# Performance work log

Hardware: AMD Instinct MI355X
Metric: run time of the kernel (lower is better)

Reference implementation:

```python
import jax, jax.numpy as jnp
import numpy as np

N_NODES = 100000
N_EDGES = 1600000
D_FEAT = 64
POS_DIM = 3
D_HID = 64


def setup_inputs() -> dict:
    key = jax.random.key(0)
    ks = jax.random.split(key, 8)
    s = lambda fan_in: 1.0 / np.sqrt(fan_in)
    x = jax.random.normal(ks[0], (N_NODES, D_FEAT), dtype=jnp.float32)
    pos = jax.random.normal(ks[1], (N_NODES, POS_DIM), dtype=jnp.float32)
    edge_index = jax.random.randint(ks[2], (2, N_EDGES), 0, N_NODES, dtype=jnp.int64)
    d_msg_in = 2 * D_FEAT + POS_DIM  # 131
    d_agg_in = 2 * D_FEAT            # 128
    return {
        "x": x,
        "edge_index": edge_index,
        "pos": pos,
        "mw1": jax.random.normal(ks[3], (d_msg_in, D_HID), dtype=jnp.float32) * s(d_msg_in),
        "mb1": jnp.zeros((D_HID,), dtype=jnp.float32),
        "mw2": jax.random.normal(ks[4], (D_HID, D_HID), dtype=jnp.float32) * s(D_HID),
        "mb2": jnp.zeros((D_HID,), dtype=jnp.float32),
        "aw1": jax.random.normal(ks[5], (d_agg_in, D_HID), dtype=jnp.float32) * s(d_agg_in),
        "ab1": jnp.zeros((D_HID,), dtype=jnp.float32),
        "aw2": jax.random.normal(ks[6], (D_HID, D_HID), dtype=jnp.float32) * s(D_HID),
        "ab2": jnp.zeros((D_HID,), dtype=jnp.float32),
    }


def reference(x, edge_index, pos, mw1, mb1, mw2, mb2, aw1, ab1, aw2, ab2):
    # flow='target_to_source': aggregation node i = edge_index[0], neighbor j = edge_index[1]
    i = edge_index[0]
    j = edge_index[1]
    # message: msg_net(cat[x_i, x_j, pos_j - pos_i])   [E, 2d+pos]
    inp = jnp.concatenate([x[i], x[j], pos[j] - pos[i]], axis=1)
    h = jax.nn.relu(inp @ mw1 + mb1)
    msg = h @ mw2 + mb2  # [E, D_HID]
    n = x.shape[0]
    # scatter-mean aggregate at node i
    msg_sum = jax.ops.segment_sum(msg, i, num_segments=n)
    cnt = jax.ops.segment_sum(jnp.ones((i.shape[0], 1), x.dtype), i, num_segments=n)
    aggr = msg_sum / jnp.maximum(cnt, 1.0)
    # update: aggr_net(cat[x, aggr])  (self_val=True)
    u = jnp.concatenate([x, aggr], axis=1)
    return jax.nn.relu(u @ aw1 + ab1) @ aw2 + ab2
```

## Files before the change

### kernel.cpp

```cpp
#include <hip/hip_runtime.h>
#include <hip/hip_fp16.h>

#define N_NODES 100000
#define N_EDGES 1600000
#define NPART 98
#define CAP   20480
#define EB    8192

typedef _Float16 half8 __attribute__((ext_vector_type(8)));
typedef float f32x4 __attribute__((ext_vector_type(4)));

#define WS_OFF   0
#define WS_PCUR  400016
#define WS_B     400528
#define WS_SJ    401040
#define WS_WCOMB 6801040
#define WS_BCOMB 6817424
#define WS_PK    6817680
#define WS_QI8   6858640
#define WS_QS    13258640
#define WS_BIN   19658640
#define WS_HM16  19658640

__global__ void k_init0(int* pcur) {
    int t = threadIdx.x;
    if (t < NPART) pcur[t] = t * CAP;
}

__global__ void __launch_bounds__(256) k_binc(const int* __restrict__ ei,
                                              const int* __restrict__ ej,
                                              int* pcur, int* __restrict__ binned) {
    __shared__ int cnt[NPART];
    __shared__ int wcur[NPART];
    int t = threadIdx.x;
    for (int q = t; q < NPART; q += 256) cnt[q] = 0;
    __syncthreads();
    int base_e = blockIdx.x * EB;
    #pragma unroll 2
    for (int it = 0; it < EB / 1024; ++it) {
        int e = base_e + it * 1024 + t * 4;
        if (e < N_EDGES) {
            int4 iv = *(const int4*)(ei + e);
            atomicAdd(&cnt[iv.x >> 10], 1);
            atomicAdd(&cnt[iv.y >> 10], 1);
            atomicAdd(&cnt[iv.z >> 10], 1);
            atomicAdd(&cnt[iv.w >> 10], 1);
        }
    }
    __syncthreads();
    for (int q = t; q < NPART; q += 256)
        wcur[q] = cnt[q] ? atomicAdd(&pcur[q], cnt[q]) : 0;
    __syncthreads();
    #pragma unroll 2
    for (int it = 0; it < EB / 1024; ++it) {
        int e = base_e + it * 1024 + t * 4;
        if (e < N_EDGES) {
            int4 iv = *(const int4*)(ei + e);
            int4 jv = *(const int4*)(ej + e);
            int a, p;
            p = iv.x >> 10; a = atomicAdd(&wcur[p], 1);
            if (a < (p + 1) * CAP) binned[a] = ((iv.x & 1023) << 17) | jv.x;
            p = iv.y >> 10; a = atomicAdd(&wcur[p], 1);
            if (a < (p + 1) * CAP) binned[a] = ((iv.y & 1023) << 17) | jv.y;
            p = iv.z >> 10; a = atomicAdd(&wcur[p], 1);
            if (a < (p + 1) * CAP) binned[a] = ((iv.z & 1023) << 17) | jv.z;
            p = iv.w >> 10; a = atomicAdd(&wcur[p], 1);
            if (a < (p + 1) * CAP) binned[a] = ((iv.w & 1023) << 17) | jv.w;
        }
    }
}

__global__ void k_scanB(const int* __restrict__ pcur, int* B) {
    __shared__ int s[128];
    int t = threadIdx.x;
    int c = 0;
    if (t < NPART) c = min(pcur[t] - t * CAP, CAP);
    s[t] = c;
    __syncthreads();
    for (int o = 1; o < 128; o <<= 1) {
        int a = (t >= o) ? s[t - o] : 0;
        __syncthreads();
        s[t] += a;
        __syncthreads();
    }
    if (t < NPART) B[t] = s[t] - c;
    if (t == NPART - 1) B[NPART] = s[t];
}

__global__ void __launch_bounds__(256) k_fill3(const int* __restrict__ binned,
                                               const int* __restrict__ B,
                                               int* __restrict__ off,
                                               int* __restrict__ sj) {
    __shared__ int hist[1024];
    __shared__ int tsum[256];
    int p = blockIdx.x, t = threadIdx.x;
    int b0g = B[p];
    int cnt_p = B[p + 1] - b0g;
    const int* src = binned + p * CAP;

    #pragma unroll
    for (int q = 0; q < 4; ++q) hist[t * 4 + q] = 0;
    __syncthreads();
    for (int e = t; e < cnt_p; e += 256) atomicAdd(&hist[src[e] >> 17], 1);
    __syncthreads();

    int b0 = hist[t * 4], b1 = hist[t * 4 + 1], b2 = hist[t * 4 + 2], b3 = hist[t * 4 + 3];
    int c1 = b0, c2 = c1 + b1, c3 = c2 + b2, tot = c3 + b3;
    tsum[t] = tot;
    __syncthreads();
    for (int o = 1; o < 256; o <<= 1) {
        int a = (t >= o) ? tsum[t - o] : 0;
        __syncthreads();
        tsum[t] += a;
        __syncthreads();
    }
    int tex = tsum[t] - tot;
    hist[t * 4]     = tex;
    hist[t * 4 + 1] = tex + c1;
    hist[t * 4 + 2] = tex + c2;
    hist[t * 4 + 3] = tex + c3;
    __syncthreads();

    int lo = p * 1024;
    #pragma unroll
    for (int q = 0; q < 4; ++q) {
        int n = t * 4 + q, g = lo + n;
        if (g < N_NODES) off[g] = b0g + hist[n];
    }
    if (p == NPART - 1 && t == 0) off[N_NODES] = B[NPART];
    __syncthreads();

    for (int e = t; e < cnt_p; e += 256) {
        int v = src[e];
        int slot = atomicAdd(&hist[v >> 17], 1);
        sj[b0g + slot] = v & 0x1FFFF;
    }
}

__global__ void k_wcomb(const float* __restrict__ mw2, const float* __restrict__ mb2,
                        const float* __restrict__ aw1, float* wcomb, float* bcomb) {
    int o = blockIdx.x * blockDim.x + threadIdx.x;
    if (o < 64 * 64) {
        int c = o >> 6, k = o & 63;
        float s = 0.f;
        #pragma unroll 8
        for (int a = 0; a < 64; ++a) s += mw2[c * 64 + a] * aw1[(64 + a) * 64 + k];
        wcomb[o] = s;
    } else if (o < 64 * 64 + 64) {
        int k = o - 64 * 64;
        float s = 0.f;
        #pragma unroll 8
        for (int a = 0; a < 64; ++a) s += mb2[a] * aw1[(64 + a) * 64 + k];
        bcomb[k] = s;
    }
}

__global__ void k_wpack(const float* __restrict__ mw1, const float* __restrict__ aw1,
                        const float* __restrict__ wcomb, const float* __restrict__ aw2,
                        _Float16* __restrict__ pk) {
    int mat = blockIdx.x;
    const float* src = (mat == 0) ? mw1 : (mat == 1) ? (mw1 + 4096)
                     : (mat == 2) ? aw1 : (mat == 3) ? wcomb : aw2;
    _Float16* dst = pk + mat * 4096;
    for (int t = threadIdx.x; t < 4096; t += 256) {
        int b_ = t & 7, l = (t >> 3) & 63, z = t >> 9;
        int kg = z & 1, nt = z >> 1;
        int k = kg * 32 + ((l >> 4) << 3) + b_;
        int n = nt * 16 + (l & 15);
        dst[t] = (_Float16)src[k * 64 + n];
    }
}

__device__ __forceinline__ half8 afrag_f32(const float* src, int row, int kg, int l) {
    const float* p = src + (size_t)row * 64 + kg * 32 + ((l >> 4) << 3);
    float4 u = *(const float4*)p;
    float4 v = *(const float4*)(p + 4);
    half8 h;
    h[0] = (_Float16)u.x; h[1] = (_Float16)u.y; h[2] = (_Float16)u.z; h[3] = (_Float16)u.w;
    h[4] = (_Float16)v.x; h[5] = (_Float16)v.y; h[6] = (_Float16)v.z; h[7] = (_Float16)v.w;
    return h;
}

__global__ void __launch_bounds__(256) k_pre(const float* __restrict__ x,
                                             const float* __restrict__ pos,
                                             const float* __restrict__ mw1,
                                             const float* __restrict__ mb1,
                                             const _Float16* __restrict__ pk,
                                             float* __restrict__ P,
                                             signed char* __restrict__ Qi8,
                                             float* __restrict__ Qs) {
    int w = threadIdx.x >> 6, l = threadIdx.x & 63;
    int m0 = blockIdx.x * 128 + w * 32;

    half8 a[2][2];
    #pragma unroll
    for (int s = 0; s < 2; ++s)
        #pragma unroll
        for (int kg = 0; kg < 2; ++kg) {
            int row = m0 + s * 16 + (l & 15);
            if (row >= N_NODES) row = N_NODES - 1;
            a[s][kg] = afrag_f32(x, row, kg, l);
        }

    f32x4 z = {0.f, 0.f, 0.f, 0.f};
    f32x4 accP[2][4], accQ[2][4];
    #pragma unroll
    for (int s = 0; s < 2; ++s)
        #pragma unroll
        for (int nt = 0; nt < 4; ++nt) { accP[s][nt] = z; accQ[s][nt] = z; }

    #pragma unroll
    for (int nt = 0; nt < 4; ++nt)
        #pragma unroll
        for (int kg = 0; kg < 2; ++kg) {
            half8 b = *(const half8*)(pk + ((nt * 2 + kg) * 64 + l) * 8);
            accP[0][nt] = __builtin_amdgcn_mfma_f32_16x16x32_f16(a[0][kg], b, accP[0][nt], 0, 0, 0);
            accP[1][nt] = __builtin_amdgcn_mfma_f32_16x16x32_f16(a[1][kg], b, accP[1][nt], 0, 0, 0);
        }
    const _Float16* pkb = pk + 4096;
    #pragma unroll
    for (int nt = 0; nt < 4; ++nt)
        #pragma unroll
        for (int kg = 0; kg < 2; ++kg) {
            half8 b = *(const half8*)(pkb + ((nt * 2 + kg) * 64 + l) * 8);
            accQ[0][nt] = __builtin_amdgcn_mfma_f32_16x16x32_f16(a[0][kg], b, accQ[0][nt], 0, 0, 0);
            accQ[1][nt] = __builtin_amdgcn_mfma_f32_16x16x32_f16(a[1][kg], b, accQ[1][nt], 0, 0, 0);
        }

    int col = l & 15;
    float wx[4], wy[4], wz[4], bb[4];
    #pragma unroll
    for (int nt = 0; nt < 4; ++nt) {
        int n = nt * 16 + col;
        wx[nt] = mw1[128 * 64 + n];
        wy[nt] = mw1[129 * 64 + n];
        wz[nt] = mw1[130 * 64 + n];
        bb[nt] = mb1[n];
    }
    #pragma unroll
    for (int s = 0; s < 2; ++s)
        #pragma unroll
        for (int r = 0; r < 4; ++r) {
            int m = m0 + s * 16 + ((l >> 4) << 2) + r;
            if (m >= N_NODES) continue;
            float px = pos[3 * m], py = pos[3 * m + 1], pz = pos[3 * m + 2];
            float qn[4];
            #pragma unroll
            for (int nt = 0; nt < 4; ++nt) {
                int n = nt * 16 + col;
                float pd = px * wx[nt] + py * wy[nt] + pz * wz[nt];
                P[(size_t)m * 64 + n] = accP[s][nt][r] + bb[nt] - pd;
                qn[nt] = accQ[s][nt][r] + pd;
            }
            float mx = fmaxf(fmaxf(fabsf(qn[0]), fabsf(qn[1])),
                             fmaxf(fabsf(qn[2]), fabsf(qn[3])));
            #pragma unroll
            for (int d = 1; d < 16; d <<= 1) mx = fmaxf(mx, __shfl_xor(mx, d, 64));
            float inv = (mx > 0.f) ? 127.f / mx : 0.f;
            #pragma unroll
            for (int nt = 0; nt < 4; ++nt)
                Qi8[(size_t)m * 64 + nt * 16 + col] = (signed char)(int)rintf(qn[nt] * inv);
            if (col == 0) Qs[m] = mx * (1.f / 127.f);
        }
}

#define G1(k) int j##k = __builtin_amdgcn_readlane(jv, G + k); \
              float b##k = (float)Qi8[(size_t)j##k * 64 + lane]; \
              float s##k = Qs[j##k];
#define G2(k) r += (G + k < m) ? fmaxf(fmaf(b##k, s##k, Pv), 0.f) : 0.f;

template<int G>
__device__ __forceinline__ float grp16(int jv, int m, float Pv, int lane,
                                       const signed char* __restrict__ Qi8,
                                       const float* __restrict__ Qs) {
    if (G >= m) return 0.f;
    G1(0)  G1(1)  G1(2)  G1(3)  G1(4)  G1(5)  G1(6)  G1(7)
    G1(8)  G1(9)  G1(10) G1(11) G1(12) G1(13) G1(14) G1(15)
    float r = 0.f;
    G2(0)  G2(1)  G2(2)  G2(3)  G2(4)  G2(5)  G2(6)  G2(7)
    G2(8)  G2(9)  G2(10) G2(11) G2(12) G2(13) G2(14) G2(15)
    return r;
}

__global__ void __launch_bounds__(256) k_c1(const signed char* __restrict__ Qi8,
                                            const float* __restrict__ Qs,
                                            const int* __restrict__ off,
                                            const int* __restrict__ sj,
                                            const float* __restrict__ Phm,
                                            _Float16* __restrict__ hm16) {
    int wave = threadIdx.x >> 6, lane = threadIdx.x & 63;
    int node = blockIdx.x * 4 + wave;
    if (node >= N_NODES) return;
    float Pv = __builtin_nontemporal_load(&Phm[(size_t)node * 64 + lane]);
    int o0 = off[node], o1 = off[node + 1];
    int dg = o1 - o0;
    float acc = 0.f;
    for (int base = o0; base < o1; base += 64) {
        int m = min(64, o1 - base);
        int jv = (lane < m) ? __builtin_nontemporal_load(&sj[base + lane]) : 0;
        acc += grp16<0>(jv, m, Pv, lane, Qi8, Qs);
        acc += grp16<16>(jv, m, Pv, lane, Qi8, Qs);
        acc += grp16<32>(jv, m, Pv, lane, Qi8, Qs);
        acc += grp16<48>(jv, m, Pv, lane, Qi8, Qs);
    }
    _Float16 hv = (_Float16)((dg > 0) ? acc / (float)dg : 0.f);
    __builtin_nontemporal_store(hv, &hm16[(size_t)node * 64 + lane]);
}

__global__ void __launch_bounds__(256) k_c2(const float* __restrict__ x,
                                            const _Float16* __restrict__ hm16,
                                            const _Float16* __restrict__ pk,
                                            const float* __restrict__ ab1,
                                            const float* __restrict__ bcomb,
                                            const float* __restrict__ ab2,
                                            const int* __restrict__ off,
                                            float* __restrict__ out) {
    __shared__ _Float16 lsh[4][2][16][64];
    int w = threadIdx.x >> 6, l = threadIdx.x & 63;
    int m0 = blockIdx.x * 128 + w * 32;
    int col = l & 15;

    f32x4 z = {0.f, 0.f, 0.f, 0.f};
    f32x4 acc[2][4];
    #pragma unroll
    for (int s = 0; s < 2; ++s)
        #pragma unroll
        for (int nt = 0; nt < 4; ++nt) acc[s][nt] = z;

    {
        half8 a[2][2];
        #pragma unroll
        for (int s = 0; s < 2; ++s)
            #pragma unroll
            for (int kg = 0; kg < 2; ++kg) {
                int row = m0 + s * 16 + (l & 15);
                if (row >= N_NODES) row = N_NODES - 1;
                a[s][kg] = afrag_f32(x, row, kg, l);
            }
        const _Float16* pk1 = pk + 2 * 4096;
        #pragma unroll
        for (int nt = 0; nt < 4; ++nt)
            #pragma unroll
            for (int kg = 0; kg < 2; ++kg) {
                half8 b = *(const half8*)(pk1 + ((nt * 2 + kg) * 64 + l) * 8);
                acc[0][nt] = __builtin_amdgcn_mfma_f32_16x16x32_f16(a[0][kg], b, acc[0][nt], 0, 0, 0);
                acc[1][nt] = __builtin_amdgcn_mfma_f32_16x16x32_f16(a[1][kg], b, acc[1][nt], 0, 0, 0);
            }
    }
    {
        half8 a[2][2];
        #pragma unroll
        for (int s = 0; s < 2; ++s)
            #pragma unroll
            for (int kg = 0; kg < 2; ++kg) {
                int row = m0 + s * 16 + (l & 15);
                if (row >= N_NODES) row = N_NODES - 1;
                a[s][kg] = *(const half8*)(hm16 + (size_t)row * 64 + kg * 32 + ((l >> 4) << 3));
            }
        const _Float16* pk2 = pk + 3 * 4096;
        #pragma unroll
        for (int nt = 0; nt < 4; ++nt)
            #pragma unroll
            for (int kg = 0; kg < 2; ++kg) {
                half8 b = *(const half8*)(pk2 + ((nt * 2 + kg) * 64 + l) * 8);
                acc[0][nt] = __builtin_amdgcn_mfma_f32_16x16x32_f16(a[0][kg], b, acc[0][nt], 0, 0, 0);
                acc[1][nt] = __builtin_amdgcn_mfma_f32_16x16x32_f16(a[1][kg], b, acc[1][nt], 0, 0, 0);
            }
    }

    float a1n[4], bcn[4];
    #pragma unroll
    for (int nt = 0; nt < 4; ++nt) {
        int n = nt * 16 + col;
        a1n[nt] = ab1[n];
        bcn[nt] = bcomb[n];
    }
    #pragma unroll
    for (int s = 0; s < 2; ++s)
        #pragma unroll
        for (int r = 0; r < 4; ++r) {
            int row = ((l >> 4) << 2) + r;
            int m = m0 + s * 16 + row;
            int dg = (m < N_NODES) ? (off[m + 1] - off[m]) : 0;
            #pragma unroll
            for (int nt = 0; nt < 4; ++nt) {
                int n = nt * 16 + col;
                float v = acc[s][nt][r] + a1n[nt] + ((dg > 0) ? bcn[nt] : 0.f);
                v = fmaxf(v, 0.f);
                lsh[w][s][row][n ^ ((row & 7) << 3)] = (_Float16)v;
            }
        }
    __syncthreads();

    f32x4 acc2[2][4];
    #pragma unroll
    for (int s = 0; s < 2; ++s)
        #pragma unroll
        for (int nt = 0; nt < 4; ++nt) acc2[s][nt] = z;
    {
        half8 a[2][2];
        #pragma unroll
        for (int s = 0; s < 2; ++s)
            #pragma unroll
            for (int kg = 0; kg < 2; ++kg) {
                int rr = l & 15;
                int c0 = (kg * 32 + ((l >> 4) << 3)) ^ ((rr & 7) << 3);
                a[s][kg] = *(const half8*)&lsh[w][s][rr][c0];
            }
        const _Float16* pk3 = pk + 4 * 4096;
        #pragma unroll
        for (int nt = 0; nt < 4; ++nt)
            #pragma unroll
            for (int kg = 0; kg < 2; ++kg) {
                half8 b = *(const half8*)(pk3 + ((nt * 2 + kg) * 64 + l) * 8);
                acc2[0][nt] = __builtin_amdgcn_mfma_f32_16x16x32_f16(a[0][kg], b, acc2[0][nt], 0, 0, 0);
                acc2[1][nt] = __builtin_amdgcn_mfma_f32_16x16x32_f16(a[1][kg], b, acc2[1][nt], 0, 0, 0);
            }
    }

    float a2n[4];
    #pragma unroll
    for (int nt = 0; nt < 4; ++nt) a2n[nt] = ab2[nt * 16 + col];
    #pragma unroll
    for (int s = 0; s < 2; ++s)
        #pragma unroll
        for (int r = 0; r < 4; ++r) {
            int m = m0 + s * 16 + ((l >> 4) << 2) + r;
            if (m >= N_NODES) continue;
            #pragma unroll
            for (int nt = 0; nt < 4; ++nt)
                out[(size_t)m * 64 + nt * 16 + col] = acc2[s][nt][r] + a2n[nt];
        }
}

extern "C" void kernel_launch(void* const* d_in, const int* in_sizes, int n_in,
                              void* d_out, int out_size, void* d_ws, size_t ws_size,
                              hipStream_t stream) {
    const float* x   = (const float*)d_in[0];
    const int*   ei  = (const int*)d_in[1];
    const int*   ej  = ((const int*)d_in[1]) + N_EDGES;
    const float* pos = (const float*)d_in[2];
    const float* mw1 = (const float*)d_in[3];
    const float* mb1 = (const float*)d_in[4];
    const float* mw2 = (const float*)d_in[5];
    const float* mb2 = (const float*)d_in[6];
    const float* aw1 = (const float*)d_in[7];
    const float* ab1 = (const float*)d_in[8];
    const float* aw2 = (const float*)d_in[9];
    const float* ab2 = (const float*)d_in[10];

    char* ws = (char*)d_ws;
    int*         off    = (int*)(ws + WS_OFF);
    int*         pcur   = (int*)(ws + WS_PCUR);
    int*         B      = (int*)(ws + WS_B);
    int*         sj     = (int*)(ws + WS_SJ);
    float*       wcomb  = (float*)(ws + WS_WCOMB);
    float*       bcomb  = (float*)(ws + WS_BCOMB);
    _Float16*    pk     = (_Float16*)(ws + WS_PK);
    signed char* Qi8    = (signed char*)(ws + WS_QI8);
    float*       Qs     = (float*)(ws + WS_QS);
    int*         binned = (int*)(ws + WS_BIN);
    _Float16*    hm16   = (_Float16*)(ws + WS_HM16);
    float*       out    = (float*)d_out;

    const int NBT = (N_NODES + 127) / 128;
    const int NBB = (N_EDGES + EB - 1) / EB;
    hipLaunchKernelGGL(k_init0, dim3(1), dim3(128), 0, stream, pcur);
    hipLaunchKernelGGL(k_binc,  dim3(NBB), dim3(256), 0, stream, ei, ej, pcur, binned);
    hipLaunchKernelGGL(k_scanB, dim3(1), dim3(128), 0, stream, pcur, B);
    hipLaunchKernelGGL(k_fill3, dim3(NPART), dim3(256), 0, stream, binned, B, off, sj);
    hipLaunchKernelGGL(k_wcomb, dim3(17), dim3(256), 0, stream, mw2, mb2, aw1, wcomb, bcomb);
    hipLaunchKernelGGL(k_wpack, dim3(5), dim3(256), 0, stream, mw1, aw1, wcomb, aw2, pk);
    hipLaunchKernelGGL(k_pre,   dim3(NBT), dim3(256), 0, stream, x, pos, mw1, mb1, pk, out, Qi8, Qs);
    hipLaunchKernelGGL(k_c1,    dim3((N_NODES + 3) / 4), dim3(256), 0, stream,
                       Qi8, Qs, off, sj, out, hm16);
    hipLaunchKernelGGL(k_c2,    dim3(NBT), dim3(256), 0, stream,
                       x, hm16, pk, ab1, bcomb, ab2, off, out);
}
```

Before: 168.1 us.

## Merge setup kernels, fuse binning with node precompute, switch Q to fp16

Folds init, weight combine and weight pack into one setup kernel. Edge binning and the per-node P/Q precompute now run as one launch with disjoint block ranges, and the partition scan moves into the fill kernel. The int8 Q with per-row scale is replaced by plain fp16 Q, which removes the quantisation reductions and the scale lookup in the gather. The cost is twice the bytes per gathered neighbour row in the edge aggregation kernel.

```diff
diff --git a/kernel.cpp b/kernel.cpp
--- a/kernel.cpp
+++ b/kernel.cpp
@@ -6,6 +6,8 @@
 #define NPART 98
 #define CAP   20480
 #define EB    8192
+#define NBB   ((N_EDGES + EB - 1) / EB)
+#define NBT   ((N_NODES + 127) / 128)
 
 typedef _Float16 half8 __attribute__((ext_vector_type(8)));
 typedef float f32x4 __attribute__((ext_vector_type(4)));
@@ -14,160 +16,54 @@
 #define WS_PCUR  400016
 #define WS_B     400528
 #define WS_SJ    401040
-#define WS_WCOMB 6801040
 #define WS_BCOMB 6817424
 #define WS_PK    6817680
-#define WS_QI8   6858640
-#define WS_QS    13258640
+#define WS_Q     6858640
 #define WS_BIN   19658640
 #define WS_HM16  19658640
 
-__global__ void k_init0(int* pcur) {
-    int t = threadIdx.x;
-    if (t < NPART) pcur[t] = t * CAP;
-}
-
-__global__ void __launch_bounds__(256) k_binc(const int* __restrict__ ei,
-                                              const int* __restrict__ ej,
-                                              int* pcur, int* __restrict__ binned) {
-    __shared__ int cnt[NPART];
-    __shared__ int wcur[NPART];
-    int t = threadIdx.x;
-    for (int q = t; q < NPART; q += 256) cnt[q] = 0;
-    __syncthreads();
-    int base_e = blockIdx.x * EB;
-    #pragma unroll 2
-    for (int it = 0; it < EB / 1024; ++it) {
-        int e = base_e + it * 1024 + t * 4;
-        if (e < N_EDGES) {
-            int4 iv = *(const int4*)(ei + e);
-            atomicAdd(&cnt[iv.x >> 10], 1);
-            atomicAdd(&cnt[iv.y >> 10], 1);
-            atomicAdd(&cnt[iv.z >> 10], 1);
-            atomicAdd(&cnt[iv.w >> 10], 1);
-        }
-    }
-    __syncthreads();
-    for (int q = t; q < NPART; q += 256)
-        wcur[q] = cnt[q] ? atomicAdd(&pcur[q], cnt[q]) : 0;
-    __syncthreads();
-    #pragma unroll 2
-    for (int it = 0; it < EB / 1024; ++it) {
-        int e = base_e + it * 1024 + t * 4;
-        if (e < N_EDGES) {
-            int4 iv = *(const int4*)(ei + e);
-            int4 jv = *(const int4*)(ej + e);
-            int a, p;
-            p = iv.x >> 10; a = atomicAdd(&wcur[p], 1);
-            if (a < (p + 1) * CAP) binned[a] = ((iv.x & 1023) << 17) | jv.x;
-            p = iv.y >> 10; a = atomicAdd(&wcur[p], 1);
-            if (a < (p + 1) * CAP) binned[a] = ((iv.y & 1023) << 17) | jv.y;
-            p = iv.z >> 10; a = atomicAdd(&wcur[p], 1);
-            if (a < (p + 1) * CAP) binned[a] = ((iv.z & 1023) << 17) | jv.z;
-            p = iv.w >> 10; a = atomicAdd(&wcur[p], 1);
-            if (a < (p + 1) * CAP) binned[a] = ((iv.w & 1023) << 17) | jv.w;
-        }
-    }
-}
-
-__global__ void k_scanB(const int* __restrict__ pcur, int* B) {
-    __shared__ int s[128];
-    int t = threadIdx.x;
-    int c = 0;
-    if (t < NPART) c = min(pcur[t] - t * CAP, CAP);
-    s[t] = c;
-    __syncthreads();
-    for (int o = 1; o < 128; o <<= 1) {
-        int a = (t >= o) ? s[t - o] : 0;
-        __syncthreads();
-        s[t] += a;
-        __syncthreads();
-    }
-    if (t < NPART) B[t] = s[t] - c;
-    if (t == NPART - 1) B[NPART] = s[t];
-}
-
-__global__ void __launch_bounds__(256) k_fill3(const int* __restrict__ binned,
-                                               const int* __restrict__ B,
-                                               int* __restrict__ off,
-                                               int* __restrict__ sj) {
-    __shared__ int hist[1024];
-    __shared__ int tsum[256];
-    int p = blockIdx.x, t = threadIdx.x;
-    int b0g = B[p];
-    int cnt_p = B[p + 1] - b0g;
-    const int* src = binned + p * CAP;
-
-    #pragma unroll
-    for (int q = 0; q < 4; ++q) hist[t * 4 + q] = 0;
-    __syncthreads();
-    for (int e = t; e < cnt_p; e += 256) atomicAdd(&hist[src[e] >> 17], 1);
-    __syncthreads();
-
-    int b0 = hist[t * 4], b1 = hist[t * 4 + 1], b2 = hist[t * 4 + 2], b3 = hist[t * 4 + 3];
-    int c1 = b0, c2 = c1 + b1, c3 = c2 + b2, tot = c3 + b3;
-    tsum[t] = tot;
-    __syncthreads();
-    for (int o = 1; o < 256; o <<= 1) {
-        int a = (t >= o) ? tsum[t - o] : 0;
-        __syncthreads();
-        tsum[t] += a;
-        __syncthreads();
-    }
-    int tex = tsum[t] - tot;
-    hist[t * 4]     = tex;
-    hist[t * 4 + 1] = tex + c1;
-    hist[t * 4 + 2] = tex + c2;
-    hist[t * 4 + 3] = tex + c3;
-    __syncthreads();
-
-    int lo = p * 1024;
-    #pragma unroll
-    for (int q = 0; q < 4; ++q) {
-        int n = t * 4 + q, g = lo + n;
-        if (g < N_NODES) off[g] = b0g + hist[n];
-    }
-    if (p == NPART - 1 && t == 0) off[N_NODES] = B[NPART];
-    __syncthreads();
-
-    for (int e = t; e < cnt_p; e += 256) {
-        int v = src[e];
-        int slot = atomicAdd(&hist[v >> 17], 1);
-        sj[b0g + slot] = v & 0x1FFFF;
-    }
-}
-
-__global__ void k_wcomb(const float* __restrict__ mw2, const float* __restrict__ mb2,
-                        const float* __restrict__ aw1, float* wcomb, float* bcomb) {
-    int o = blockIdx.x * blockDim.x + threadIdx.x;
-    if (o < 64 * 64) {
-        int c = o >> 6, k = o & 63;
-        float s = 0.f;
-        #pragma unroll 8
-        for (int a = 0; a < 64; ++a) s += mw2[c * 64 + a] * aw1[(64 + a) * 64 + k];
-        wcomb[o] = s;
-    } else if (o < 64 * 64 + 64) {
-        int k = o - 64 * 64;
-        float s = 0.f;
-        #pragma unroll 8
-        for (int a = 0; a < 64; ++a) s += mb2[a] * aw1[(64 + a) * 64 + k];
-        bcomb[k] = s;
-    }
-}
-
-__global__ void k_wpack(const float* __restrict__ mw1, const float* __restrict__ aw1,
-                        const float* __restrict__ wcomb, const float* __restrict__ aw2,
-                        _Float16* __restrict__ pk) {
-    int mat = blockIdx.x;
-    const float* src = (mat == 0) ? mw1 : (mat == 1) ? (mw1 + 4096)
-                     : (mat == 2) ? aw1 : (mat == 3) ? wcomb : aw2;
-    _Float16* dst = pk + mat * 4096;
-    for (int t = threadIdx.x; t < 4096; t += 256) {
-        int b_ = t & 7, l = (t >> 3) & 63, z = t >> 9;
-        int kg = z & 1, nt = z >> 1;
-        int k = kg * 32 + ((l >> 4) << 3) + b_;
-        int n = nt * 16 + (l & 15);
-        dst[t] = (_Float16)src[k * 64 + n];
+__global__ void __launch_bounds__(256) k_setup(const float* __restrict__ mw1,
+                                               const float* __restrict__ mw2,
+                                               const float* __restrict__ mb2,
+                                               const float* __restrict__ aw1,
+                                               const float* __restrict__ aw2,
+                                               _Float16* __restrict__ pk,
+                                               float* __restrict__ bcomb,
+                                               int* __restrict__ pcur) {
+    __shared__ float wc[4096];
+    int blk = blockIdx.x, t = threadIdx.x;
+    if (blk < 5) {
+        const float* src;
+        if (blk == 3) {
+            for (int o = t; o < 4096; o += 256) {
+                int c = o >> 6, k = o & 63;
+                float s = 0.f;
+                #pragma unroll 8
+                for (int a = 0; a < 64; ++a) s += mw2[c * 64 + a] * aw1[(64 + a) * 64 + k];
+                wc[o] = s;
+            }
+            __syncthreads();
+            src = wc;
+        } else {
+            src = (blk == 0) ? mw1 : (blk == 1) ? (mw1 + 4096)
+                : (blk == 2) ? aw1 : aw2;
+        }
+        _Float16* dst = pk + blk * 4096;
+        for (int o = t; o < 4096; o += 256) {
+            int b_ = o & 7, l = (o >> 3) & 63, z = o >> 9;
+            int kg = z & 1, nt = z >> 1;
+            int k = kg * 32 + ((l >> 4) << 3) + b_;
+            int n = nt * 16 + (l & 15);
+            dst[o] = (_Float16)src[k * 64 + n];
+        }
+    } else {
+        if (t < 64) {
+            float s = 0.f;
+            #pragma unroll 8
+            for (int a = 0; a < 64; ++a) s += mb2[a] * aw1[(64 + a) * 64 + t];
+            bcomb[t] = s;
+        }
+        if (t < 128) pcur[t] = t * CAP;
     }
 }
 
@@ -181,16 +77,60 @@
     return h;
 }
 
-__global__ void __launch_bounds__(256) k_pre(const float* __restrict__ x,
-                                             const float* __restrict__ pos,
-                                             const float* __restrict__ mw1,
-                                             const float* __restrict__ mb1,
-                                             const _Float16* __restrict__ pk,
-                                             float* __restrict__ P,
-                                             signed char* __restrict__ Qi8,
-                                             float* __restrict__ Qs) {
-    int w = threadIdx.x >> 6, l = threadIdx.x & 63;
-    int m0 = blockIdx.x * 128 + w * 32;
+__global__ void __launch_bounds__(256) k_binpre(const int* __restrict__ ei,
+                                                const int* __restrict__ ej,
+                                                int* pcur, int* __restrict__ binned,
+                                                const float* __restrict__ x,
+                                                const float* __restrict__ pos,
+                                                const float* __restrict__ mw1,
+                                                const float* __restrict__ mb1,
+                                                const _Float16* __restrict__ pk,
+                                                float* __restrict__ P,
+                                                _Float16* __restrict__ Q16) {
+    __shared__ int cnt[NPART];
+    __shared__ int wcur[NPART];
+    int t = threadIdx.x;
+    if (blockIdx.x < NBB) {
+        for (int q = t; q < NPART; q += 256) cnt[q] = 0;
+        __syncthreads();
+        int base_e = blockIdx.x * EB;
+        #pragma unroll 2
+        for (int it = 0; it < EB / 1024; ++it) {
+            int e = base_e + it * 1024 + t * 4;
+            if (e < N_EDGES) {
+                int4 iv = *(const int4*)(ei + e);
+                atomicAdd(&cnt[iv.x >> 10], 1);
+                atomicAdd(&cnt[iv.y >> 10], 1);
+                atomicAdd(&cnt[iv.z >> 10], 1);
+                atomicAdd(&cnt[iv.w >> 10], 1);
+            }
+        }
+        __syncthreads();
+        for (int q = t; q < NPART; q += 256)
+            wcur[q] = cnt[q] ? atomicAdd(&pcur[q], cnt[q]) : 0;
+        __syncthreads();
+        #pragma unroll 2
+        for (int it = 0; it < EB / 1024; ++it) {
+            int e = base_e + it * 1024 + t * 4;
+            if (e < N_EDGES) {
+                int4 iv = *(const int4*)(ei + e);
+                int4 jv = *(const int4*)(ej + e);
+                int a, p;
+                p = iv.x >> 10; a = atomicAdd(&wcur[p], 1);
+                if (a < (p + 1) * CAP) binned[a] = ((iv.x & 1023) << 17) | jv.x;
+                p = iv.y >> 10; a = atomicAdd(&wcur[p], 1);
+                if (a < (p + 1) * CAP) binned[a] = ((iv.y & 1023) << 17) | jv.y;
+                p = iv.z >> 10; a = atomicAdd(&wcur[p], 1);
+                if (a < (p + 1) * CAP) binned[a] = ((iv.z & 1023) << 17) | jv.z;
+                p = iv.w >> 10; a = atomicAdd(&wcur[p], 1);
+                if (a < (p + 1) * CAP) binned[a] = ((iv.w & 1023) << 17) | jv.w;
+            }
+        }
+        return;
+    }
+    int bid = blockIdx.x - NBB;
+    int w = t >> 6, l = t & 63;
+    int m0 = bid * 128 + w * 32;
 
     half8 a[2][2];
     #pragma unroll
@@ -244,35 +184,90 @@
             int m = m0 + s * 16 + ((l >> 4) << 2) + r;
             if (m >= N_NODES) continue;
             float px = pos[3 * m], py = pos[3 * m + 1], pz = pos[3 * m + 2];
-            float qn[4];
             #pragma unroll
             for (int nt = 0; nt < 4; ++nt) {
                 int n = nt * 16 + col;
                 float pd = px * wx[nt] + py * wy[nt] + pz * wz[nt];
                 P[(size_t)m * 64 + n] = accP[s][nt][r] + bb[nt] - pd;
-                qn[nt] = accQ[s][nt][r] + pd;
-            }
-            float mx = fmaxf(fmaxf(fabsf(qn[0]), fabsf(qn[1])),
-                             fmaxf(fabsf(qn[2]), fabsf(qn[3])));
-            #pragma unroll
-            for (int d = 1; d < 16; d <<= 1) mx = fmaxf(mx, __shfl_xor(mx, d, 64));
-            float inv = (mx > 0.f) ? 127.f / mx : 0.f;
-            #pragma unroll
-            for (int nt = 0; nt < 4; ++nt)
-                Qi8[(size_t)m * 64 + nt * 16 + col] = (signed char)(int)rintf(qn[nt] * inv);
-            if (col == 0) Qs[m] = mx * (1.f / 127.f);
-        }
+                Q16[(size_t)m * 64 + n] = (_Float16)(accQ[s][nt][r] + pd);
+            }
+        }
+}
+
+__global__ void __launch_bounds__(256) k_fill3s(const int* __restrict__ binned,
+                                                const int* __restrict__ pcur,
+                                                int* __restrict__ off,
+                                                int* __restrict__ sj) {
+    __shared__ int bs[128];
+    __shared__ int hist[1024];
+    __shared__ int tsum[256];
+    int p = blockIdx.x, t = threadIdx.x;
+
+    int c = 0;
+    if (t < 128) {
+        if (t < NPART) c = min(pcur[t] - t * CAP, CAP);
+        bs[t] = c;
+    }
+    __syncthreads();
+    for (int o = 1; o < 128; o <<= 1) {
+        int a = 0;
+        if (t < 128 && t >= o) a = bs[t - o];
+        __syncthreads();
+        if (t < 128) bs[t] += a;
+        __syncthreads();
+    }
+    int cp = min(pcur[p] - p * CAP, CAP);
+    int b0g = bs[p] - cp;
+    int cnt_p = cp;
+    int total = bs[NPART - 1];
+    const int* src = binned + p * CAP;
+
+    #pragma unroll
+    for (int q = 0; q < 4; ++q) hist[t * 4 + q] = 0;
+    __syncthreads();
+    for (int e = t; e < cnt_p; e += 256) atomicAdd(&hist[src[e] >> 17], 1);
+    __syncthreads();
+
+    int b0 = hist[t * 4], b1 = hist[t * 4 + 1], b2 = hist[t * 4 + 2], b3 = hist[t * 4 + 3];
+    int c1 = b0, c2 = c1 + b1, c3 = c2 + b2, tot = c3 + b3;
+    tsum[t] = tot;
+    __syncthreads();
+    for (int o = 1; o < 256; o <<= 1) {
+        int a = (t >= o) ? tsum[t - o] : 0;
+        __syncthreads();
+        tsum[t] += a;
+        __syncthreads();
+    }
+    int tex = tsum[t] - tot;
+    hist[t * 4]     = tex;
+    hist[t * 4 + 1] = tex + c1;
+    hist[t * 4 + 2] = tex + c2;
+    hist[t * 4 + 3] = tex + c3;
+    __syncthreads();
+
+    int lo = p * 1024;
+    #pragma unroll
+    for (int q = 0; q < 4; ++q) {
+        int n = t * 4 + q, g = lo + n;
+        if (g < N_NODES) off[g] = b0g + hist[n];
+    }
+    if (p == NPART - 1 && t == 0) off[N_NODES] = total;
+    __syncthreads();
+
+    for (int e = t; e < cnt_p; e += 256) {
+        int v = src[e];
+        int slot = atomicAdd(&hist[v >> 17], 1);
+        sj[b0g + slot] = v & 0x1FFFF;
+    }
 }
 
 #define G1(k) int j##k = __builtin_amdgcn_readlane(jv, G + k); \
-              float b##k = (float)Qi8[(size_t)j##k * 64 + lane]; \
-              float s##k = Qs[j##k];
-#define G2(k) r += (G + k < m) ? fmaxf(fmaf(b##k, s##k, Pv), 0.f) : 0.f;
+              float v##k = (float)Q16[(size_t)j##k * 64 + lane];
+#define G2(k) r += (G + k < m) ? fmaxf(Pv + v##k, 0.f) : 0.f;
 
 template<int G>
 __device__ __forceinline__ float grp16(int jv, int m, float Pv, int lane,
-                                       const signed char* __restrict__ Qi8,
-                                       const float* __restrict__ Qs) {
+                                       const _Float16* __restrict__ Q16) {
     if (G >= m) return 0.f;
     G1(0)  G1(1)  G1(2)  G1(3)  G1(4)  G1(5)  G1(6)  G1(7)
     G1(8)  G1(9)  G1(10) G1(11) G1(12) G1(13) G1(14) G1(15)
@@ -282,8 +277,7 @@
     return r;
 }
 
-__global__ void __launch_bounds__(256) k_c1(const signed char* __restrict__ Qi8,
-                                            const float* __restrict__ Qs,
+__global__ void __launch_bounds__(256) k_c1(const _Float16* __restrict__ Q16,
                                             const int* __restrict__ off,
                                             const int* __restrict__ sj,
                                             const float* __restrict__ Phm,
@@ -298,10 +292,10 @@
     for (int base = o0; base < o1; base += 64) {
         int m = min(64, o1 - base);
         int jv = (lane < m) ? __builtin_nontemporal_load(&sj[base + lane]) : 0;
-        acc += grp16<0>(jv, m, Pv, lane, Qi8, Qs);
-        acc += grp16<16>(jv, m, Pv, lane, Qi8, Qs);
-        acc += grp16<32>(jv, m, Pv, lane, Qi8, Qs);
-        acc += grp16<48>(jv, m, Pv, lane, Qi8, Qs);
+        acc += grp16<0>(jv, m, Pv, lane, Q16);
+        acc += grp16<16>(jv, m, Pv, lane, Q16);
+        acc += grp16<32>(jv, m, Pv, lane, Q16);
+        acc += grp16<48>(jv, m, Pv, lane, Q16);
     }
     _Float16 hv = (_Float16)((dg > 0) ? acc / (float)dg : 0.f);
     __builtin_nontemporal_store(hv, &hm16[(size_t)node * 64 + lane]);
@@ -450,30 +444,24 @@
     const float* ab2 = (const float*)d_in[10];
 
     char* ws = (char*)d_ws;
-    int*         off    = (int*)(ws + WS_OFF);
-    int*         pcur   = (int*)(ws + WS_PCUR);
-    int*         B      = (int*)(ws + WS_B);
-    int*         sj     = (int*)(ws + WS_SJ);
-    float*       wcomb  = (float*)(ws + WS_WCOMB);
-    float*       bcomb  = (float*)(ws + WS_BCOMB);
-    _Float16*    pk     = (_Float16*)(ws + WS_PK);
-    signed char* Qi8    = (signed char*)(ws + WS_QI8);
-    float*       Qs     = (float*)(ws + WS_QS);
-    int*         binned = (int*)(ws + WS_BIN);
-    _Float16*    hm16   = (_Float16*)(ws + WS_HM16);
-    float*       out    = (float*)d_out;
-
-    const int NBT = (N_NODES + 127) / 128;
-    const int NBB = (N_EDGES + EB - 1) / EB;
-    hipLaunchKernelGGL(k_init0, dim3(1), dim3(128), 0, stream, pcur);
-    hipLaunchKernelGGL(k_binc,  dim3(NBB), dim3(256), 0, stream, ei, ej, pcur, binned);
-    hipLaunchKernelGGL(k_scanB, dim3(1), dim3(128), 0, stream, pcur, B);
-    hipLaunchKernelGGL(k_fill3, dim3(NPART), dim3(256), 0, stream, binned, B, off, sj);
-    hipLaunchKernelGGL(k_wcomb, dim3(17), dim3(256), 0, stream, mw2, mb2, aw1, wcomb, bcomb);
-    hipLaunchKernelGGL(k_wpack, dim3(5), dim3(256), 0, stream, mw1, aw1, wcomb, aw2, pk);
-    hipLaunchKernelGGL(k_pre,   dim3(NBT), dim3(256), 0, stream, x, pos, mw1, mb1, pk, out, Qi8, Qs);
-    hipLaunchKernelGGL(k_c1,    dim3((N_NODES + 3) / 4), dim3(256), 0, stream,
-                       Qi8, Qs, off, sj, out, hm16);
-    hipLaunchKernelGGL(k_c2,    dim3(NBT), dim3(256), 0, stream,
+    int*       off    = (int*)(ws + WS_OFF);
+    int*       pcur   = (int*)(ws + WS_PCUR);
+    int*       sj     = (int*)(ws + WS_SJ);
+    float*     bcomb  = (float*)(ws + WS_BCOMB);
+    _Float16*  pk     = (_Float16*)(ws + WS_PK);
+    _Float16*  Q16    = (_Float16*)(ws + WS_Q);
+    int*       binned = (int*)(ws + WS_BIN);
+    _Float16*  hm16   = (_Float16*)(ws + WS_HM16);
+    float*     out    = (float*)d_out;
+
+    hipLaunchKernelGGL(k_setup,  dim3(6), dim3(256), 0, stream,
+                       mw1, mw2, mb2, aw1, aw2, pk, bcomb, pcur);
+    hipLaunchKernelGGL(k_binpre, dim3(NBB + NBT), dim3(256), 0, stream,
+                       ei, ej, pcur, binned, x, pos, mw1, mb1, pk, out, Q16);
+    hipLaunchKernelGGL(k_fill3s, dim3(NPART), dim3(256), 0, stream,
+                       binned, pcur, off, sj);
+    hipLaunchKernelGGL(k_c1,     dim3((N_NODES + 3) / 4), dim3(256), 0, stream,
+                       Q16, off, sj, out, hm16);
+    hipLaunchKernelGGL(k_c2,     dim3(NBT), dim3(256), 0, stream,
                        x, hm16, pk, ab1, bcomb, ab2, off, out);
 }
```

Result: faster. 162.4 us (-3.4%).
